# Kernel optimization log

Measured on AMD Instinct MI355X. Metric: run time of the kernel, lower is better.

The kernel has to match this reference:

```python
import jax, jax.numpy as jnp
import numpy as np

C = 512  # channels
B, S = 8, 2048


def setup_inputs() -> dict:
    key = jax.random.key(0)
    ks = jax.random.split(key, 8)
    x = jax.random.normal(ks[0], (B, S, C), dtype=jnp.float32)
    eigenvalues = jax.random.normal(ks[1], (B, S), dtype=jnp.float32)
    init = 1.0 / np.sqrt(C)
    Wq = jax.random.normal(ks[2], (C, C), dtype=jnp.float32) * init
    bq = jnp.zeros((C,), dtype=jnp.float32)
    Wk = jax.random.normal(ks[3], (C, C), dtype=jnp.float32) * init
    bk = jnp.zeros((C,), dtype=jnp.float32)
    Wv = jax.random.normal(ks[4], (C, C), dtype=jnp.float32) * init
    bv = jnp.zeros((C,), dtype=jnp.float32)
    return {"x": x, "eigenvalues": eigenvalues, "Wq": Wq, "bq": bq,
            "Wk": Wk, "bk": bk, "Wv": Wv, "bv": bv}


def reference(x, eigenvalues, Wq, bq, Wk, bk, Wv, bv):
    # torch nn.Linear: y = x @ W^T + b
    scale = 1.0 / np.sqrt(x.shape[-1])
    Q = jnp.einsum('bsc,dc->bsd', x, Wq) + bq
    K = jnp.einsum('bsc,dc->bsd', x, Wk) + bk
    V = jnp.einsum('bsc,dc->bsd', x, Wv) + bv
    # scores: [B, S(query), S(key)]
    scores = jnp.einsum('bqd,bkd->bqk', Q, K) * scale
    eigen_weight = jax.nn.sigmoid(eigenvalues)          # [B, S]
    scores = scores * eigen_weight[:, None, :]          # scale per key position
    attn = jax.nn.softmax(scores, axis=-1)
    return jnp.einsum('bqk,bkd->bqd', attn, V)
```

## Files before the change

kernel.cpp:

```cpp
#include <hip/hip_runtime.h>

typedef unsigned short u16;
using bf16x8 = __attribute__((ext_vector_type(8))) short;
using f32x4  = __attribute__((ext_vector_type(4))) float;

__device__ __forceinline__ u16 f2b(float f) {
    __bf16 h = (__bf16)f;
    return __builtin_bit_cast(unsigned short, h);
}
__device__ __forceinline__ float b2f(u16 u) {
    return (float)__builtin_bit_cast(__bf16, u);
}
__device__ __forceinline__ void gload16(const u16* g, const u16* l) {
    __builtin_amdgcn_global_load_lds(
        (const __attribute__((address_space(1))) unsigned int*)g,
        (__attribute__((address_space(3))) unsigned int*)l, 16, 0, 0);
}

template<int MODE, int NBLK>
__global__ __launch_bounds__(512, 2)
void gemm8(const u16* __restrict__ A, const u16* __restrict__ B,
           void* __restrict__ Cv, const float* __restrict__ aux,
           float* __restrict__ rowsum,
           int K, int lda, int ldb, int ldc,
           long strA, long strB, long strC, long strAux, long strRS)
{
    constexpr int BR = NBLK * 64;
    constexpr int BROUND = BR / 64;
    __shared__ __align__(16) u16 sA[2][256 * 64];
    __shared__ __align__(16) u16 sB[2][BR * 64];

    const int tid  = threadIdx.x;
    const int lane = tid & 63;
    const int wave = tid >> 6;
    const int wm = wave >> 2, wn = wave & 3;
    const int l16 = lane & 15, qld = lane >> 4;

    const int gx = gridDim.x, gy = gridDim.y;
    const int nxy = gx * gy;
    int li = blockIdx.y * gx + blockIdx.x;
    li = (li & 7) * (nxy >> 3) + (li >> 3);
    const int bx = li % gx, by = li / gx;
    const int bn0 = bx * BR, bm0 = by * 256;
    const long z = blockIdx.z;

    const u16* Ab = A + z * strA + (long)bm0 * lda;
    const u16* Bb = B + z * strB + (long)bn0 * ldb;
    const float* auxp = aux + z * strAux;

    const u16* srcA[4];
    const u16* srcB[BROUND];
#pragma unroll
    for (int i = 0; i < 4; ++i) {
        const int ci = i * 512 + tid, row = ci >> 3, c = ci & 7;
        srcA[i] = Ab + (long)row * lda + (c ^ (row & 7)) * 8;
    }
#pragma unroll
    for (int i = 0; i < BROUND; ++i) {
        const int ci = i * 512 + tid, row = ci >> 3, c = ci & 7;
        srcB[i] = Bb + (long)row * ldb + (c ^ (row & 7)) * 8;
    }
    const int wch = (tid & ~63) * 8;

#define STAGE_A2(sl, kc, i0) do { \
    gload16(srcA[i0] + (kc),     &sA[sl][(i0) * 4096 + wch]); \
    gload16(srcA[i0 + 1] + (kc), &sA[sl][(i0 + 1) * 4096 + wch]); } while (0)
#define STAGE_B(sl, kc) do { \
    _Pragma("unroll") \
    for (int i = 0; i < BROUND; ++i) \
        gload16(srcB[i] + (kc), &sB[sl][i * 4096 + wch]); } while (0)

    f32x4 acc[8][NBLK] = {};
    const int NT = K >> 6;

    auto rdA = [&](int s, int mf, int kh) -> bf16x8 {
        const int row = wm * 128 + mf * 16 + l16;
        int byte_off = row * 128 + (kh * 32 + qld * 8) * 2;
        byte_off ^= (row & 7) << 4;
        return *(const bf16x8*)((const char*)&sA[s][0] + byte_off);
    };
    auto rdB = [&](int s, int n, int kh) -> bf16x8 {
        const int row = wn * (NBLK * 16) + n * 16 + l16;
        int byte_off = row * 128 + (kh * 32 + qld * 8) * 2;
        byte_off ^= (row & 7) << 4;
        return *(const bf16x8*)((const char*)&sB[s][0] + byte_off);
    };

#define MFMA_HALF(base) do { \
    __builtin_amdgcn_s_setprio(1); \
    _Pragma("unroll") \
    for (int j = 0; j < 4; ++j) \
        _Pragma("unroll") \
        for (int n = 0; n < NBLK; ++n) \
            acc[(base) + j][n] = __builtin_amdgcn_mfma_f32_16x16x32_bf16(afr[j], bfr[n], acc[(base) + j][n], 0, 0, 0); \
    __builtin_amdgcn_s_setprio(0); } while (0)

#define BAR()   asm volatile("s_barrier" ::: "memory")
#define LGKM0() do { asm volatile("s_waitcnt lgkmcnt(0)" ::: "memory"); \
                     __builtin_amdgcn_sched_barrier(0); } while (0)

    STAGE_A2(0, 0, 0); STAGE_A2(0, 0, 2);
    STAGE_B(0, 0);
    STAGE_B(1, 64);
    asm volatile("s_waitcnt vmcnt(%0)" :: "i"(BROUND) : "memory");
    __builtin_amdgcn_sched_barrier(0);
    BAR();

    for (int t = 0; t < NT; ++t) {
        const int s = t & 1, s1 = s ^ 1;
        bf16x8 afr[4], bfr[NBLK];

#pragma unroll
        for (int j = 0; j < 4; ++j) afr[j] = rdA(s, j, 0);
#pragma unroll
        for (int n = 0; n < NBLK; ++n) bfr[n] = rdB(s, n, 0);
        if (t + 1 < NT) STAGE_A2(s1, (t + 1) * 64, 0);
        BAR(); LGKM0();
        MFMA_HALF(0);
        BAR();

#pragma unroll
        for (int j = 0; j < 4; ++j) afr[j] = rdA(s, 4 + j, 0);
        if (t + 1 < NT) STAGE_A2(s1, (t + 1) * 64, 2);
        BAR(); LGKM0();
        MFMA_HALF(4);
        BAR();

#pragma unroll
        for (int j = 0; j < 4; ++j) afr[j] = rdA(s, j, 1);
#pragma unroll
        for (int n = 0; n < NBLK; ++n) bfr[n] = rdB(s, n, 1);
        BAR(); LGKM0();
        MFMA_HALF(0);
        BAR();

#pragma unroll
        for (int j = 0; j < 4; ++j) afr[j] = rdA(s, 4 + j, 1);
        if (t + 2 < NT) STAGE_B(s, (t + 2) * 64);
        BAR(); LGKM0();
        MFMA_HALF(4);
        if (t + 2 < NT) asm volatile("s_waitcnt vmcnt(%0)" :: "i"(BROUND) : "memory");
        else            asm volatile("s_waitcnt vmcnt(0)" ::: "memory");
        __builtin_amdgcn_sched_barrier(0);
        BAR();
    }
#undef STAGE_A2
#undef STAGE_B
#undef MFMA_HALF
#undef BAR
#undef LGKM0

    const int rg = lane >> 4;
    const int orow0 = bm0 + wm * 128;
    const int ocol0 = bn0 + wn * (NBLK * 16);

    if constexpr (MODE == 0) {
        u16* Co = (u16*)Cv + z * strC;
        float bias[NBLK];
#pragma unroll
        for (int n = 0; n < NBLK; ++n) bias[n] = auxp[ocol0 + n * 16 + l16];
#pragma unroll
        for (int mf = 0; mf < 8; ++mf)
#pragma unroll
            for (int n = 0; n < NBLK; ++n) {
                const int col = ocol0 + n * 16 + l16;
#pragma unroll
                for (int r = 0; r < 4; ++r) {
                    const int row = orow0 + mf * 16 + rg * 4 + r;
                    Co[(long)row * ldc + col] = f2b(acc[mf][n][r] + bias[n]);
                }
            }
    } else if constexpr (MODE == 2) {
        u16* Co = (u16*)Cv + z * strC;
        float* rsp = rowsum + z * strRS;
        float wkn[NBLK];
#pragma unroll
        for (int n = 0; n < NBLK; ++n) wkn[n] = auxp[ocol0 + n * 16 + l16];
#pragma unroll
        for (int mf = 0; mf < 8; ++mf)
#pragma unroll
            for (int r = 0; r < 4; ++r) {
                const int row = orow0 + mf * 16 + rg * 4 + r;
                float partial = 0.f;
#pragma unroll
                for (int n = 0; n < NBLK; ++n) {
                    const int col = ocol0 + n * 16 + l16;
                    const float p = exp2f(acc[mf][n][r] * wkn[n]);
                    const u16 pb = f2b(p);
                    Co[(long)row * ldc + col] = pb;
                    partial += b2f(pb);
                }
                partial += __shfl_xor(partial, 1);
                partial += __shfl_xor(partial, 2);
                partial += __shfl_xor(partial, 4);
                partial += __shfl_xor(partial, 8);
                if (l16 == 0) atomicAdd(&rsp[row], partial);
            }
    } else {
        float* Co = (float*)Cv + z * strC;
#pragma unroll
        for (int mf = 0; mf < 8; ++mf)
#pragma unroll
            for (int r = 0; r < 4; ++r) {
                const int row = orow0 + mf * 16 + rg * 4 + r;
                const float inv = 1.0f / auxp[row];
#pragma unroll
                for (int n = 0; n < NBLK; ++n) {
                    const int col = ocol0 + n * 16 + l16;
                    Co[(long)row * ldc + col] = acc[mf][n][r] * inv;
                }
            }
    }
}

__global__ void cvt_bf16(const float* __restrict__ in, u16* __restrict__ out, int n4) {
    const int i = blockIdx.x * 256 + threadIdx.x;
    if (i >= n4) return;
    const float4 f = ((const float4*)in)[i];
    ushort4 o;
    o.x = f2b(f.x); o.y = f2b(f.y); o.z = f2b(f.z); o.w = f2b(f.w);
    ((ushort4*)out)[i] = o;
}

__global__ void wk_kernel(const float* __restrict__ eig, float* __restrict__ wk, int n) {
    const int i = blockIdx.x * 256 + threadIdx.x;
    if (i >= n) return;
    const float s = 1.0f / (1.0f + expf(-eig[i]));
    wk[i] = s * (float)(1.4426950408889634 / 22.627416997969522);
}

__global__ __launch_bounds__(256)
void transpose_v(const u16* __restrict__ Vq, u16* __restrict__ Vt) {
    __shared__ u16 t[64][65];
    const int tid = threadIdx.x;
    const int d0  = blockIdx.x * 64;
    const int bs0 = blockIdx.y * 64;
#pragma unroll
    for (int i = 0; i < 16; ++i) {
        const int idx = i * 256 + tid;
        const int r = idx >> 6, c = idx & 63;
        t[r][c] = Vq[(long)(bs0 + r) * 1536 + d0 + c];
    }
    __syncthreads();
    const long b = bs0 >> 11;
    const int s0 = bs0 & 2047;
#pragma unroll
    for (int i = 0; i < 16; ++i) {
        const int idx = i * 256 + tid;
        const int dch = idx >> 6, ss = idx & 63;
        Vt[(b * 512 + d0 + dch) * 2048 + s0 + ss] = t[ss][dch];
    }
}

extern "C" void kernel_launch(void* const* d_in, const int* in_sizes, int n_in,
                              void* d_out, int out_size, void* d_ws, size_t ws_size,
                              hipStream_t stream) {
    const float* x  = (const float*)d_in[0];
    const float* ev = (const float*)d_in[1];
    const float* Wq = (const float*)d_in[2];
    const float* bq = (const float*)d_in[3];
    const float* Wk = (const float*)d_in[4];
    const float* bk = (const float*)d_in[5];
    const float* Wv = (const float*)d_in[6];
    const float* bv = (const float*)d_in[7];
    float* out = (float*)d_out;

    char* ws = (char*)d_ws;
    u16*   P      = (u16*)(ws);
    u16*   xb     = (u16*)(ws + (64ul << 20));
    u16*   qkvC   = (u16*)(ws + (80ul << 20));
    u16*   Vt     = (u16*)(ws + (128ul << 20));
    u16*   Wb     = (u16*)(ws + (144ul << 20));
    float* biasb  = (float*)(ws + (146ul << 20));
    float* wk     = (float*)(ws + (146ul << 20) + 65536);
    float* rowsum = (float*)(ws + (146ul << 20) + 131072);

    cvt_bf16<<<dim3(8192), dim3(256), 0, stream>>>(x, xb, 2097152);
    cvt_bf16<<<dim3(256),  dim3(256), 0, stream>>>(Wq, Wb,          65536);
    cvt_bf16<<<dim3(256),  dim3(256), 0, stream>>>(Wk, Wb + 262144, 65536);
    cvt_bf16<<<dim3(256),  dim3(256), 0, stream>>>(Wv, Wb + 524288, 65536);
    hipMemcpyAsync(biasb,        bq, 512 * 4, hipMemcpyDeviceToDevice, stream);
    hipMemcpyAsync(biasb + 512,  bk, 512 * 4, hipMemcpyDeviceToDevice, stream);
    hipMemcpyAsync(biasb + 1024, bv, 512 * 4, hipMemcpyDeviceToDevice, stream);
    wk_kernel<<<dim3(64), dim3(256), 0, stream>>>(ev, wk, 16384);
    hipMemsetAsync(rowsum, 0, 65536, stream);

    gemm8<0, 2><<<dim3(12, 64, 1), dim3(512), 0, stream>>>(
        xb, Wb, qkvC, biasb, nullptr,
        512, 512, 512, 1536,
        0L, 0L, 0L, 0L, 0L);

    transpose_v<<<dim3(8, 256), dim3(256), 0, stream>>>(qkvC + 1024, Vt);

    gemm8<2, 4><<<dim3(8, 8, 8), dim3(512), 0, stream>>>(
        qkvC, qkvC + 512, P, wk, rowsum,
        512, 1536, 1536, 2048,
        3145728L, 3145728L, 4194304L, 2048L, 2048L);

    gemm8<3, 2><<<dim3(4, 8, 8), dim3(512), 0, stream>>>(
        P, Vt, out, rowsum, nullptr,
        2048, 2048, 2048, 512,
        4194304L, 1048576L, 1048576L, 2048L, 0L);
}
```

Before: 272.0 us.

## Fuse QK^T, exp and PV into one attention kernel without materializing P

Measured after the change: 294.2 us. 1.08x slower.

```diff
diff --git a/kernel.cpp b/kernel.cpp
--- a/kernel.cpp
+++ b/kernel.cpp
@@ -16,19 +16,152 @@
         (const __attribute__((address_space(1))) unsigned int*)g,
         (__attribute__((address_space(3))) unsigned int*)l, 16, 0, 0);
 }
-
-template<int MODE, int NBLK>
+__device__ __forceinline__ f32x4 mfma16(bf16x8 a, bf16x8 b, f32x4 c) {
+    return __builtin_amdgcn_mfma_f32_16x16x32_bf16(a, b, c, 0, 0, 0);
+}
+
+__global__ __launch_bounds__(1024, 4)
+void attn_fused(const u16* __restrict__ qkv, const u16* __restrict__ Vt,
+                const float* __restrict__ wk, float* __restrict__ out)
+{
+    __shared__ __align__(16) u16 Qs[64 * 512];
+    __shared__ __align__(16) u16 Ps[64 * 256];
+    __shared__ float rs[64];
+
+    const int tid  = threadIdx.x;
+    const int lane = tid & 63;
+    const int w    = tid >> 6;
+    const int l16  = lane & 15, g = lane >> 4;
+
+    const int lid = blockIdx.x;
+    const long z  = lid & 7;
+    const int qt  = lid >> 3;
+    const long qrow0 = z * 2048 + (long)qt * 64;
+
+    if (tid < 64) rs[tid] = 0.f;
+
+#pragma unroll
+    for (int i = 0; i < 4; ++i) {
+        const int ci = i * 1024 + tid;
+        const int q = ci >> 6, c = ci & 63;
+        const u16* src = qkv + (qrow0 + q) * 1536 + (c ^ (q & 7)) * 8;
+        gload16(src, &Qs[(i * 1024 + (tid & ~63)) * 8]);
+    }
+
+    f32x4 oacc[4][2] = {};
+    float rsum0 = 0.f, rsum1 = 0.f, rsum2 = 0.f, rsum3 = 0.f;
+
+    const u16* Kbase = qkv + z * 2048 * 1536 + 512;
+    const u16* Vbase = Vt + z * 512 * 2048;
+    const float* wkb = wk + z * 2048;
+
+    asm volatile("s_waitcnt vmcnt(0)" ::: "memory");
+    __syncthreads();
+
+    for (int ch = 0; ch < 8; ++ch) {
+        const int c0 = ch * 256;
+
+        f32x4 sacc0 = {}, sacc1 = {}, sacc2 = {}, sacc3 = {};
+        const u16* Kp = Kbase + (long)(c0 + 16 * w + l16) * 1536 + g * 8;
+#pragma unroll
+        for (int kf = 0; kf < 16; ++kf) {
+            const bf16x8 a = *(const bf16x8*)(Kp + kf * 32);
+#pragma unroll
+            for (int nf = 0; nf < 4; ++nf) {
+                const int q = nf * 16 + l16;
+                const int byt = q * 1024 + ((kf * 64 + g * 16) ^ ((q & 7) << 4));
+                const bf16x8 b = *(const bf16x8*)((const char*)Qs + byt);
+                if (nf == 0) sacc0 = mfma16(a, b, sacc0);
+                else if (nf == 1) sacc1 = mfma16(a, b, sacc1);
+                else if (nf == 2) sacc2 = mfma16(a, b, sacc2);
+                else sacc3 = mfma16(a, b, sacc3);
+            }
+        }
+
+        const float* wkp = wkb + c0 + 16 * w + g * 4;
+        const float wk0 = wkp[0], wk1 = wkp[1], wk2 = wkp[2], wk3 = wkp[3];
+#pragma unroll
+        for (int nf = 0; nf < 4; ++nf) {
+            const f32x4 sv = (nf == 0) ? sacc0 : (nf == 1) ? sacc1 : (nf == 2) ? sacc2 : sacc3;
+            const u16 p0 = f2b(exp2f(sv[0] * wk0));
+            const u16 p1 = f2b(exp2f(sv[1] * wk1));
+            const u16 p2 = f2b(exp2f(sv[2] * wk2));
+            const u16 p3 = f2b(exp2f(sv[3] * wk3));
+            const float part = b2f(p0) + b2f(p1) + b2f(p2) + b2f(p3);
+            if (nf == 0) rsum0 += part;
+            else if (nf == 1) rsum1 += part;
+            else if (nf == 2) rsum2 += part;
+            else rsum3 += part;
+            const int q = nf * 16 + l16;
+            const int byt = q * 512 + ((32 * w + 8 * g) ^ ((q & 7) << 4));
+            uint2 pk;
+            pk.x = (unsigned)p0 | ((unsigned)p1 << 16);
+            pk.y = (unsigned)p2 | ((unsigned)p3 << 16);
+            *(uint2*)((char*)Ps + byt) = pk;
+        }
+        __syncthreads();
+
+        const u16* Vp = Vbase + (long)(w * 32 + l16) * 2048 + c0 + g * 8;
+#pragma unroll
+        for (int kf = 0; kf < 8; ++kf) {
+            bf16x8 pa0, pa1, pa2, pa3;
+            {
+                const int q0 = l16;
+                pa0 = *(const bf16x8*)((const char*)Ps + q0 * 512 + ((kf * 64 + g * 16) ^ ((q0 & 7) << 4)));
+                const int q1 = 16 + l16;
+                pa1 = *(const bf16x8*)((const char*)Ps + q1 * 512 + ((kf * 64 + g * 16) ^ ((q1 & 7) << 4)));
+                const int q2 = 32 + l16;
+                pa2 = *(const bf16x8*)((const char*)Ps + q2 * 512 + ((kf * 64 + g * 16) ^ ((q2 & 7) << 4)));
+                const int q3 = 48 + l16;
+                pa3 = *(const bf16x8*)((const char*)Ps + q3 * 512 + ((kf * 64 + g * 16) ^ ((q3 & 7) << 4)));
+            }
+#pragma unroll
+            for (int nf = 0; nf < 2; ++nf) {
+                const bf16x8 b = *(const bf16x8*)(Vp + nf * 16 * 2048 + kf * 32);
+                oacc[0][nf] = mfma16(pa0, b, oacc[0][nf]);
+                oacc[1][nf] = mfma16(pa1, b, oacc[1][nf]);
+                oacc[2][nf] = mfma16(pa2, b, oacc[2][nf]);
+                oacc[3][nf] = mfma16(pa3, b, oacc[3][nf]);
+            }
+        }
+        __syncthreads();
+    }
+
+    {
+        float v0 = rsum0, v1 = rsum1, v2 = rsum2, v3 = rsum3;
+        v0 += __shfl_xor(v0, 16); v0 += __shfl_xor(v0, 32);
+        v1 += __shfl_xor(v1, 16); v1 += __shfl_xor(v1, 32);
+        v2 += __shfl_xor(v2, 16); v2 += __shfl_xor(v2, 32);
+        v3 += __shfl_xor(v3, 16); v3 += __shfl_xor(v3, 32);
+        if (g == 0) {
+            atomicAdd(&rs[l16], v0);
+            atomicAdd(&rs[16 + l16], v1);
+            atomicAdd(&rs[32 + l16], v2);
+            atomicAdd(&rs[48 + l16], v3);
+        }
+    }
+    __syncthreads();
+
+#pragma unroll
+    for (int qf = 0; qf < 4; ++qf)
+#pragma unroll
+        for (int r = 0; r < 4; ++r) {
+            const int row = qf * 16 + g * 4 + r;
+            const float inv = 1.0f / rs[row];
+#pragma unroll
+            for (int nf = 0; nf < 2; ++nf)
+                out[(qrow0 + row) * 512 + w * 32 + nf * 16 + l16] = oacc[qf][nf][r] * inv;
+        }
+}
+
 __global__ __launch_bounds__(512, 2)
-void gemm8(const u16* __restrict__ A, const u16* __restrict__ B,
-           void* __restrict__ Cv, const float* __restrict__ aux,
-           float* __restrict__ rowsum,
-           int K, int lda, int ldb, int ldc,
-           long strA, long strB, long strC, long strAux, long strRS)
+void proj_gemm(const u16* __restrict__ A, const u16* __restrict__ B,
+               u16* __restrict__ C, const float* __restrict__ bias,
+               int K, int lda, int ldb, int ldc)
 {
-    constexpr int BR = NBLK * 64;
-    constexpr int BROUND = BR / 64;
+    constexpr int BROUND = 2;
     __shared__ __align__(16) u16 sA[2][256 * 64];
-    __shared__ __align__(16) u16 sB[2][BR * 64];
+    __shared__ __align__(16) u16 sB[2][128 * 64];
 
     const int tid  = threadIdx.x;
     const int lane = tid & 63;
@@ -41,12 +174,10 @@
     int li = blockIdx.y * gx + blockIdx.x;
     li = (li & 7) * (nxy >> 3) + (li >> 3);
     const int bx = li % gx, by = li / gx;
-    const int bn0 = bx * BR, bm0 = by * 256;
-    const long z = blockIdx.z;
-
-    const u16* Ab = A + z * strA + (long)bm0 * lda;
-    const u16* Bb = B + z * strB + (long)bn0 * ldb;
-    const float* auxp = aux + z * strAux;
+    const int bn0 = bx * 128, bm0 = by * 256;
+
+    const u16* Ab = A + (long)bm0 * lda;
+    const u16* Bb = B + (long)bn0 * ldb;
 
     const u16* srcA[4];
     const u16* srcB[BROUND];
@@ -70,7 +201,7 @@
     for (int i = 0; i < BROUND; ++i) \
         gload16(srcB[i] + (kc), &sB[sl][i * 4096 + wch]); } while (0)
 
-    f32x4 acc[8][NBLK] = {};
+    f32x4 acc[8][2] = {};
     const int NT = K >> 6;
 
     auto rdA = [&](int s, int mf, int kh) -> bf16x8 {
@@ -80,7 +211,7 @@
         return *(const bf16x8*)((const char*)&sA[s][0] + byte_off);
     };
     auto rdB = [&](int s, int n, int kh) -> bf16x8 {
-        const int row = wn * (NBLK * 16) + n * 16 + l16;
+        const int row = wn * 32 + n * 16 + l16;
         int byte_off = row * 128 + (kh * 32 + qld * 8) * 2;
         byte_off ^= (row & 7) << 4;
         return *(const bf16x8*)((const char*)&sB[s][0] + byte_off);
@@ -91,8 +222,8 @@
     _Pragma("unroll") \
     for (int j = 0; j < 4; ++j) \
         _Pragma("unroll") \
-        for (int n = 0; n < NBLK; ++n) \
-            acc[(base) + j][n] = __builtin_amdgcn_mfma_f32_16x16x32_bf16(afr[j], bfr[n], acc[(base) + j][n], 0, 0, 0); \
+        for (int n = 0; n < 2; ++n) \
+            acc[(base) + j][n] = mfma16(afr[j], bfr[n], acc[(base) + j][n]); \
     __builtin_amdgcn_s_setprio(0); } while (0)
 
 #define BAR()   asm volatile("s_barrier" ::: "memory")
@@ -108,12 +239,12 @@
 
     for (int t = 0; t < NT; ++t) {
         const int s = t & 1, s1 = s ^ 1;
-        bf16x8 afr[4], bfr[NBLK];
+        bf16x8 afr[4], bfr[2];
 
 #pragma unroll
         for (int j = 0; j < 4; ++j) afr[j] = rdA(s, j, 0);
 #pragma unroll
-        for (int n = 0; n < NBLK; ++n) bfr[n] = rdB(s, n, 0);
+        for (int n = 0; n < 2; ++n) bfr[n] = rdB(s, n, 0);
         if (t + 1 < NT) STAGE_A2(s1, (t + 1) * 64, 0);
         BAR(); LGKM0();
         MFMA_HALF(0);
@@ -129,7 +260,7 @@
 #pragma unroll
         for (int j = 0; j < 4; ++j) afr[j] = rdA(s, j, 1);
 #pragma unroll
-        for (int n = 0; n < NBLK; ++n) bfr[n] = rdB(s, n, 1);
+        for (int n = 0; n < 2; ++n) bfr[n] = rdB(s, n, 1);
         BAR(); LGKM0();
         MFMA_HALF(0);
         BAR();
@@ -152,65 +283,22 @@
 
     const int rg = lane >> 4;
     const int orow0 = bm0 + wm * 128;
-    const int ocol0 = bn0 + wn * (NBLK * 16);
-
-    if constexpr (MODE == 0) {
-        u16* Co = (u16*)Cv + z * strC;
-        float bias[NBLK];
-#pragma unroll
-        for (int n = 0; n < NBLK; ++n) bias[n] = auxp[ocol0 + n * 16 + l16];
-#pragma unroll
-        for (int mf = 0; mf < 8; ++mf)
-#pragma unroll
-            for (int n = 0; n < NBLK; ++n) {
-                const int col = ocol0 + n * 16 + l16;
-#pragma unroll
-                for (int r = 0; r < 4; ++r) {
-                    const int row = orow0 + mf * 16 + rg * 4 + r;
-                    Co[(long)row * ldc + col] = f2b(acc[mf][n][r] + bias[n]);
-                }
-            }
-    } else if constexpr (MODE == 2) {
-        u16* Co = (u16*)Cv + z * strC;
-        float* rsp = rowsum + z * strRS;
-        float wkn[NBLK];
-#pragma unroll
-        for (int n = 0; n < NBLK; ++n) wkn[n] = auxp[ocol0 + n * 16 + l16];
-#pragma unroll
-        for (int mf = 0; mf < 8; ++mf)
+    const int ocol0 = bn0 + wn * 32;
+
+    float bv[2];
+#pragma unroll
+    for (int n = 0; n < 2; ++n) bv[n] = bias[ocol0 + n * 16 + l16];
+#pragma unroll
+    for (int mf = 0; mf < 8; ++mf)
+#pragma unroll
+        for (int n = 0; n < 2; ++n) {
+            const int col = ocol0 + n * 16 + l16;
 #pragma unroll
             for (int r = 0; r < 4; ++r) {
                 const int row = orow0 + mf * 16 + rg * 4 + r;
-                float partial = 0.f;
-#pragma unroll
-                for (int n = 0; n < NBLK; ++n) {
-                    const int col = ocol0 + n * 16 + l16;
-                    const float p = exp2f(acc[mf][n][r] * wkn[n]);
-                    const u16 pb = f2b(p);
-                    Co[(long)row * ldc + col] = pb;
-                    partial += b2f(pb);
-                }
-                partial += __shfl_xor(partial, 1);
-                partial += __shfl_xor(partial, 2);
-                partial += __shfl_xor(partial, 4);
-                partial += __shfl_xor(partial, 8);
-                if (l16 == 0) atomicAdd(&rsp[row], partial);
+                C[(long)row * ldc + col] = f2b(acc[mf][n][r] + bv[n]);
             }
-    } else {
-        float* Co = (float*)Cv + z * strC;
-#pragma unroll
-        for (int mf = 0; mf < 8; ++mf)
-#pragma unroll
-            for (int r = 0; r < 4; ++r) {
-                const int row = orow0 + mf * 16 + rg * 4 + r;
-                const float inv = 1.0f / auxp[row];
-#pragma unroll
-                for (int n = 0; n < NBLK; ++n) {
-                    const int col = ocol0 + n * 16 + l16;
-                    Co[(long)row * ldc + col] = acc[mf][n][r] * inv;
-                }
-            }
-    }
+        }
 }
 
 __global__ void cvt_bf16(const float* __restrict__ in, u16* __restrict__ out, int n4) {
@@ -266,14 +354,12 @@
     float* out = (float*)d_out;
 
     char* ws = (char*)d_ws;
-    u16*   P      = (u16*)(ws);
-    u16*   xb     = (u16*)(ws + (64ul << 20));
-    u16*   qkvC   = (u16*)(ws + (80ul << 20));
-    u16*   Vt     = (u16*)(ws + (128ul << 20));
-    u16*   Wb     = (u16*)(ws + (144ul << 20));
-    float* biasb  = (float*)(ws + (146ul << 20));
-    float* wk     = (float*)(ws + (146ul << 20) + 65536);
-    float* rowsum = (float*)(ws + (146ul << 20) + 131072);
+    u16*   xb     = (u16*)(ws);
+    u16*   qkvC   = (u16*)(ws + (16ul << 20));
+    u16*   Vt     = (u16*)(ws + (64ul << 20));
+    u16*   Wb     = (u16*)(ws + (80ul << 20));
+    float* biasb  = (float*)(ws + (82ul << 20));
+    float* wk     = (float*)(ws + (83ul << 20));
 
     cvt_bf16<<<dim3(8192), dim3(256), 0, stream>>>(x, xb, 2097152);
     cvt_bf16<<<dim3(256),  dim3(256), 0, stream>>>(Wq, Wb,          65536);
@@ -283,22 +369,11 @@
     hipMemcpyAsync(biasb + 512,  bk, 512 * 4, hipMemcpyDeviceToDevice, stream);
     hipMemcpyAsync(biasb + 1024, bv, 512 * 4, hipMemcpyDeviceToDevice, stream);
     wk_kernel<<<dim3(64), dim3(256), 0, stream>>>(ev, wk, 16384);
-    hipMemsetAsync(rowsum, 0, 65536, stream);
-
-    gemm8<0, 2><<<dim3(12, 64, 1), dim3(512), 0, stream>>>(
-        xb, Wb, qkvC, biasb, nullptr,
-        512, 512, 512, 1536,
-        0L, 0L, 0L, 0L, 0L);
+
+    proj_gemm<<<dim3(12, 64), dim3(512), 0, stream>>>(
+        xb, Wb, qkvC, biasb, 512, 512, 512, 1536);
 
     transpose_v<<<dim3(8, 256), dim3(256), 0, stream>>>(qkvC + 1024, Vt);
 
-    gemm8<2, 4><<<dim3(8, 8, 8), dim3(512), 0, stream>>>(
-        qkvC, qkvC + 512, P, wk, rowsum,
-        512, 1536, 1536, 2048,
-        3145728L, 3145728L, 4194304L, 2048L, 2048L);
-
-    gemm8<3, 2><<<dim3(4, 8, 8), dim3(512), 0, stream>>>(
-        P, Vt, out, rowsum, nullptr,
-        2048, 2048, 2048, 512,
-        4194304L, 1048576L, 1048576L, 2048L, 0L);
-}
+    attn_fused<<<dim3(256), dim3(1024), 0, stream>>>(qkvC, Vt, wk, out);
+}
```
